# Optimization experiments

Hardware: AMD Instinct MI355X
Metric: run time of the kernel (lower is better)

## Reference

```python
import jax, jax.numpy as jnp
import numpy as np

FFT_LENGTH = 2048
HOP_LENGTH = 512  # window_length // 4, window_length == fft_length


def _hann_periodic(n):
    # tf.signal.hann_window(n, periodic=True)
    return (0.5 - 0.5 * jnp.cos(2.0 * jnp.pi * jnp.arange(n) / n)).astype(jnp.float32)


def setup_inputs() -> dict:
    key = jax.random.key(0)
    k1, k2 = jax.random.split(key)
    B, F, NB = 4, 4000, FFT_LENGTH // 2 + 1
    spec_real = jax.random.normal(k1, (B, F, NB), dtype=jnp.float32)
    spec_imag = jax.random.normal(k2, (B, F, NB), dtype=jnp.float32)
    return {"spec_real": spec_real, "spec_imag": spec_imag}


def reference(spec_real, spec_imag) -> jnp.ndarray:
    fft_length, hop = FFT_LENGTH, HOP_LENGTH
    B, F, _ = spec_real.shape
    window = _hann_periodic(fft_length)  # [N], window_length == fft_length so no padding

    # irfft of the complex spectrogram -> time-domain frames [B, F, N]
    frames = jnp.fft.irfft(spec_real + 1j * spec_imag, n=fft_length).astype(jnp.float32)
    windowed = window * frames  # [B, F, N]

    # overlap-and-add: output length L = (F-1)*hop + N
    L = (F - 1) * hop + fft_length
    idx = (jnp.arange(F) * hop)[:, None] + jnp.arange(fft_length)[None, :]  # [F, N]
    out = jnp.zeros((B, L), jnp.float32).at[:, idx].add(windowed)

    # librosa window_sumsquare: overlap-add of squared window, guard tiny values
    wsq = jnp.zeros((L,), jnp.float32).at[idx].add(window * window)
    tiny = jnp.float32(np.finfo(np.float32).tiny)
    window_sum = jnp.where(wsq > tiny, wsq, jnp.float32(1.0))

    y = out / window_sum
    # center=True: trim fft_length//2 on each side
    half = fft_length // 2
    return y[:, half:L - half]
```

## Files before the change

### kernel.cpp

```cpp
#include <hip/hip_runtime.h>
#include <math.h>

#define NB       1025
#define M        1024
#define FFTN     2048
#define HOP      512
#define NFRAMES  4000
#define BATCH    4
#define OUT_T    2047488
#define R_HOPS   8
#define REG_PB   501
#define ACC_N    (R_HOPS * HOP)
#define PI_F     3.14159265358979323846f

__device__ __forceinline__ float2 cmul(float2 a, float2 b) {
    return make_float2(a.x*b.x - a.y*b.y, a.x*b.y + a.y*b.x);
}
__device__ __forceinline__ int SW(int i) { return i ^ ((i >> 4) & 15); }

__device__ __forceinline__ float wsq_at(int p) {
    int u  = p + FFTN / 2;
    int fm = u >> 9;
    int n0 = u & 511;
    float wsq = 0.f;
    #pragma unroll
    for (int jj = 0; jj < 4; ++jj) {
        int fr = fm - jj;
        if (fr >= 0 && fr < NFRAMES) {
            int n = n0 + (jj << 9);
            float sw = __sinf((PI_F / (float)FFTN) * (float)n);
            float w  = sw * sw;
            wsq += w * w;
        }
    }
    const float tiny = 1.17549435e-38f;
    return (wsq > tiny) ? wsq : 1.0f;
}

template<int ST>
__device__ __forceinline__ void stage(const float2* __restrict__ src,
                                      float2* __restrict__ dst, int j,
                                      float2 w1, float2 w2, float2 w3) {
    const int Ns = 1 << (2 * ST);
    float2 v0 = src[SW(j)];
    float2 v1 = src[SW(j + 256)];
    float2 v2 = src[SW(j + 512)];
    float2 v3 = src[SW(j + 768)];
    v1 = cmul(v1, w1); v2 = cmul(v2, w2); v3 = cmul(v3, w3);
    float2 t0 = make_float2(v0.x + v2.x, v0.y + v2.y);
    float2 t1 = make_float2(v0.x - v2.x, v0.y - v2.y);
    float2 t2 = make_float2(v1.x + v3.x, v1.y + v3.y);
    float2 t3 = make_float2(v1.x - v3.x, v1.y - v3.y);
    int jm = j & (Ns - 1);
    int idxD = ((j >> (2 * ST)) << (2 * ST + 2)) + jm;
    dst[SW(idxD         )] = make_float2(t0.x + t2.x, t0.y + t2.y);
    dst[SW(idxD +     Ns)] = make_float2(t1.x - t3.y, t1.y + t3.x);
    dst[SW(idxD + 2 * Ns)] = make_float2(t0.x - t2.x, t0.y - t2.y);
    dst[SW(idxD + 3 * Ns)] = make_float2(t1.x + t3.y, t1.y - t3.x);
}

__global__ __launch_bounds__(256) void istft_region_kernel(
    const float* __restrict__ sr, const float* __restrict__ si,
    float* __restrict__ out)
{
    __shared__ float2 buf0[M];
    __shared__ float2 buf1[M];
    __shared__ float2 acc2[ACC_N / 2];

    const int blk = blockIdx.x;
    const int b   = blk / REG_PB;
    const int reg = blk - b * REG_PB;
    const int s0h = reg * R_HOPS;
    const int j   = threadIdx.x;

    #pragma unroll
    for (int q = 0; q < ACC_N / 2 / 256; ++q)
        acc2[j + q * 256] = make_float2(0.f, 0.f);

    float2 tw_pack[4];
    #pragma unroll
    for (int kk = 0; kk < 4; ++kk) {
        int k = j + kk * 256;
        float s, c;
        __sincosf(PI_F * (float)k * (1.0f / (float)M), &s, &c);
        tw_pack[kk] = make_float2(c, s);
    }
    float2 w1s[4], w2s[4], w3s[4];
    #pragma unroll
    for (int st = 1; st <= 4; ++st) {
        int Ns = 1 << (2 * st);
        int jm = j & (Ns - 1);
        float ang = (0.5f * PI_F / (float)Ns) * (float)jm;
        float s1, c1;
        __sincosf(ang, &s1, &c1);
        float2 w1 = make_float2(c1, s1);
        w1s[st-1] = w1;
        w2s[st-1] = cmul(w1, w1);
        w3s[st-1] = cmul(w2s[st-1], w1);
    }
    float wreg[4][2];
    #pragma unroll
    for (int q = 0; q < 4; ++q) {
        int n = j + q * 256;
        #pragma unroll
        for (int h = 0; h < 2; ++h) {
            int t = 2 * n + h;
            float swv = __sinf((PI_F / (float)FFTN) * (float)t);
            wreg[q][h] = swv * swv * (1.0f / 1024.0f);
        }
    }

    int f0 = s0h - 3;           if (f0 < 0)           f0 = 0;
    int f1 = s0h + R_HOPS - 1;  if (f1 > NFRAMES - 1) f1 = NFRAMES - 1;

    __syncthreads();

    float car[4], cai[4], cbr[4], cbi[4];
    {
        const size_t fb = ((size_t)b * NFRAMES + f0) * NB;
        const float* __restrict__ xr = sr + fb;
        const float* __restrict__ xi = si + fb;
        #pragma unroll
        for (int kk = 0; kk < 4; ++kk) {
            int k  = j + kk * 256;
            int mk = M - k;
            car[kk] = xr[k];  cai[kk] = xi[k];
            cbr[kk] = xr[mk]; cbi[kk] = xi[mk];
        }
    }

    for (int f = f0; f <= f1; ++f) {
        {
            float2 z[4];
            #pragma unroll
            for (int kk = 0; kk < 4; ++kk) {
                float arv = car[kk], aiv = cai[kk];
                float brv = cbr[kk], biv = cbi[kk];
                if (kk == 0 && j == 0) { aiv = 0.f; biv = 0.f; }
                float Er = 0.5f * (arv + brv), Ei = 0.5f * (aiv - biv);
                float Dr = 0.5f * (arv - brv), Di = 0.5f * (aiv + biv);
                float2 t = tw_pack[kk];
                float Or = Dr * t.x - Di * t.y;
                float Oi = Dr * t.y + Di * t.x;
                z[kk] = make_float2(Er - Oi, Ei + Or);
            }
            float2 t0 = make_float2(z[0].x + z[2].x, z[0].y + z[2].y);
            float2 t1 = make_float2(z[0].x - z[2].x, z[0].y - z[2].y);
            float2 t2 = make_float2(z[1].x + z[3].x, z[1].y + z[3].y);
            float2 t3 = make_float2(z[1].x - z[3].x, z[1].y - z[3].y);
            buf0[SW(4*j    )] = make_float2(t0.x + t2.x, t0.y + t2.y);
            buf0[SW(4*j + 1)] = make_float2(t1.x - t3.y, t1.y + t3.x);
            buf0[SW(4*j + 2)] = make_float2(t0.x - t2.x, t0.y - t2.y);
            buf0[SW(4*j + 3)] = make_float2(t1.x + t3.y, t1.y - t3.x);
        }

        float nar[4], nai[4], nbr[4], nbi[4];
        {
            int fn = (f < f1) ? (f + 1) : f1;
            const size_t fb = ((size_t)b * NFRAMES + fn) * NB;
            const float* __restrict__ xr = sr + fb;
            const float* __restrict__ xi = si + fb;
            #pragma unroll
            for (int kk = 0; kk < 4; ++kk) {
                int k  = j + kk * 256;
                int mk = M - k;
                nar[kk] = xr[k];  nai[kk] = xi[k];
                nbr[kk] = xr[mk]; nbi[kk] = xi[mk];
            }
        }

        __syncthreads();
        stage<1>(buf0, buf1, j, w1s[0], w2s[0], w3s[0]);
        __syncthreads();
        stage<2>(buf1, buf0, j, w1s[1], w2s[1], w3s[1]);
        __syncthreads();
        stage<3>(buf0, buf1, j, w1s[2], w2s[2], w3s[2]);
        __syncthreads();

        float2 v0 = buf1[SW(j)];
        float2 v1 = buf1[SW(j + 256)];
        float2 v2 = buf1[SW(j + 512)];
        float2 v3 = buf1[SW(j + 768)];
        v1 = cmul(v1, w1s[3]);
        v2 = cmul(v2, w2s[3]);
        v3 = cmul(v3, w3s[3]);
        float2 t0 = make_float2(v0.x + v2.x, v0.y + v2.y);
        float2 t1 = make_float2(v0.x - v2.x, v0.y - v2.y);
        float2 t2 = make_float2(v1.x + v3.x, v1.y + v3.y);
        float2 t3 = make_float2(v1.x - v3.x, v1.y - v3.y);
        float2 g0 = make_float2(t0.x + t2.x, t0.y + t2.y);
        float2 g1 = make_float2(t1.x - t3.y, t1.y + t3.x);
        float2 g2 = make_float2(t0.x - t2.x, t0.y - t2.y);
        float2 g3 = make_float2(t1.x + t3.y, t1.y - t3.x);

        int ofs2 = (HOP / 2) * (f - s0h);
        {
            int i2 = ofs2 + j;
            if ((unsigned)i2 < (unsigned)(ACC_N / 2)) {
                float2 a = acc2[i2];
                a.x += g0.x * wreg[0][0];  a.y += g0.y * wreg[0][1];
                acc2[i2] = a;
            }
            i2 = ofs2 + j + 256;
            if ((unsigned)i2 < (unsigned)(ACC_N / 2)) {
                float2 a = acc2[i2];
                a.x += g1.x * wreg[1][0];  a.y += g1.y * wreg[1][1];
                acc2[i2] = a;
            }
            i2 = ofs2 + j + 512;
            if ((unsigned)i2 < (unsigned)(ACC_N / 2)) {
                float2 a = acc2[i2];
                a.x += g2.x * wreg[2][0];  a.y += g2.y * wreg[2][1];
                acc2[i2] = a;
            }
            i2 = ofs2 + j + 768;
            if ((unsigned)i2 < (unsigned)(ACC_N / 2)) {
                float2 a = acc2[i2];
                a.x += g3.x * wreg[3][0];  a.y += g3.y * wreg[3][1];
                acc2[i2] = a;
            }
        }

        #pragma unroll
        for (int kk = 0; kk < 4; ++kk) {
            car[kk] = nar[kk]; cai[kk] = nai[kk];
            cbr[kk] = nbr[kk]; cbi[kk] = nbi[kk];
        }
    }

    __syncthreads();

    const float* accf = (const float*)acc2;
    const int base_u = s0h * HOP;
    float* outb = out + (size_t)b * OUT_T;
    #pragma unroll
    for (int q = 0; q < ACC_N / 256; ++q) {
        int i = j + q * 256;
        int p = base_u + i - FFTN / 2;
        if ((unsigned)p < (unsigned)OUT_T) {
            float invw = (p < 512 || p >= OUT_T - 512) ? (1.0f / wsq_at(p)) : (2.0f / 3.0f);
            outb[p] = accf[i] * invw;
        }
    }
}

extern "C" void kernel_launch(void* const* d_in, const int* in_sizes, int n_in,
                              void* d_out, int out_size, void* d_ws, size_t ws_size,
                              hipStream_t stream) {
    const float* sr = (const float*)d_in[0];
    const float* si = (const float*)d_in[1];
    float* out = (float*)d_out;
    istft_region_kernel<<<BATCH * REG_PB, 256, 0, stream>>>(sr, si, out);
}
```

Baseline: 61.30 us.

## Process two frames per iteration with in-place bit-reversed radix-4 FFT stages

The frame loop now handles two frames per pass, each in its own shared buffer. The stage-0 pack writes in digit-reversed order (rev4), so the radix-4 stages can run in place. Barriers are shared between the two frames, which cuts the per-frame synchronisation cost, and the next two frames' spectrum loads are prefetched in registers. This adds register pressure from the double prefetch and the extra in-flight data, and adds one barrier per iteration to protect buffer reuse.

```diff
diff --git a/kernel.cpp b/kernel.cpp
--- a/kernel.cpp
+++ b/kernel.cpp
@@ -18,6 +18,10 @@
 }
 __device__ __forceinline__ int SW(int i) { return i ^ ((i >> 4) & 15); }
 
+__device__ __forceinline__ int rev4(int j) {
+    return ((j & 3) << 6) | (((j >> 2) & 3) << 4) | (((j >> 4) & 3) << 2) | ((j >> 6) & 3);
+}
+
 __device__ __forceinline__ float wsq_at(int p) {
     int u  = p + FFTN / 2;
     int fm = u >> 9;
@@ -38,33 +42,106 @@
 }
 
 template<int ST>
-__device__ __forceinline__ void stage(const float2* __restrict__ src,
-                                      float2* __restrict__ dst, int j,
-                                      float2 w1, float2 w2, float2 w3) {
-    const int Ns = 1 << (2 * ST);
-    float2 v0 = src[SW(j)];
-    float2 v1 = src[SW(j + 256)];
-    float2 v2 = src[SW(j + 512)];
-    float2 v3 = src[SW(j + 768)];
+__device__ __forceinline__ void stage_ip(float2* buf, int j,
+                                         float2 w1, float2 w2, float2 w3) {
+    const int Ns   = 1 << (2 * ST);
+    const int jm   = j & (Ns - 1);
+    const int idxD = ((j >> (2 * ST)) << (2 * ST + 2)) + jm;
+    float2 v0 = buf[SW(idxD)];
+    float2 v1 = buf[SW(idxD + Ns)];
+    float2 v2 = buf[SW(idxD + 2 * Ns)];
+    float2 v3 = buf[SW(idxD + 3 * Ns)];
     v1 = cmul(v1, w1); v2 = cmul(v2, w2); v3 = cmul(v3, w3);
     float2 t0 = make_float2(v0.x + v2.x, v0.y + v2.y);
     float2 t1 = make_float2(v0.x - v2.x, v0.y - v2.y);
     float2 t2 = make_float2(v1.x + v3.x, v1.y + v3.y);
     float2 t3 = make_float2(v1.x - v3.x, v1.y - v3.y);
-    int jm = j & (Ns - 1);
-    int idxD = ((j >> (2 * ST)) << (2 * ST + 2)) + jm;
-    dst[SW(idxD         )] = make_float2(t0.x + t2.x, t0.y + t2.y);
-    dst[SW(idxD +     Ns)] = make_float2(t1.x - t3.y, t1.y + t3.x);
-    dst[SW(idxD + 2 * Ns)] = make_float2(t0.x - t2.x, t0.y - t2.y);
-    dst[SW(idxD + 3 * Ns)] = make_float2(t1.x + t3.y, t1.y - t3.x);
+    buf[SW(idxD         )] = make_float2(t0.x + t2.x, t0.y + t2.y);
+    buf[SW(idxD +     Ns)] = make_float2(t1.x - t3.y, t1.y + t3.x);
+    buf[SW(idxD + 2 * Ns)] = make_float2(t0.x - t2.x, t0.y - t2.y);
+    buf[SW(idxD + 3 * Ns)] = make_float2(t1.x + t3.y, t1.y - t3.x);
+}
+
+__device__ __forceinline__ void load_spec(const float* __restrict__ sr,
+                                          const float* __restrict__ si,
+                                          int b, int f, int j,
+                                          float* car, float* cai,
+                                          float* cbr, float* cbi) {
+    const size_t fb = ((size_t)b * NFRAMES + f) * NB;
+    const float* __restrict__ xr = sr + fb;
+    const float* __restrict__ xi = si + fb;
+    #pragma unroll
+    for (int kk = 0; kk < 4; ++kk) {
+        int k  = j + kk * 256;
+        int mk = M - k;
+        car[kk] = xr[k];  cai[kk] = xi[k];
+        cbr[kk] = xr[mk]; cbi[kk] = xi[mk];
+    }
+}
+
+__device__ __forceinline__ void pack_st0(float2* buf, int j, int R4,
+                                         const float2* tw_pack,
+                                         const float* car, const float* cai,
+                                         const float* cbr, const float* cbi) {
+    float2 z[4];
+    #pragma unroll
+    for (int kk = 0; kk < 4; ++kk) {
+        float arv = car[kk], aiv = cai[kk];
+        float brv = cbr[kk], biv = cbi[kk];
+        if (kk == 0 && j == 0) { aiv = 0.f; biv = 0.f; }
+        float Er = 0.5f * (arv + brv), Ei = 0.5f * (aiv - biv);
+        float Dr = 0.5f * (arv - brv), Di = 0.5f * (aiv + biv);
+        float2 t = tw_pack[kk];
+        float Or = Dr * t.x - Di * t.y;
+        float Oi = Dr * t.y + Di * t.x;
+        z[kk] = make_float2(Er - Oi, Ei + Or);
+    }
+    float2 t0 = make_float2(z[0].x + z[2].x, z[0].y + z[2].y);
+    float2 t1 = make_float2(z[0].x - z[2].x, z[0].y - z[2].y);
+    float2 t2 = make_float2(z[1].x + z[3].x, z[1].y + z[3].y);
+    float2 t3 = make_float2(z[1].x - z[3].x, z[1].y - z[3].y);
+    buf[SW(4 * R4    )] = make_float2(t0.x + t2.x, t0.y + t2.y);
+    buf[SW(4 * R4 + 1)] = make_float2(t1.x - t3.y, t1.y + t3.x);
+    buf[SW(4 * R4 + 2)] = make_float2(t0.x - t2.x, t0.y - t2.y);
+    buf[SW(4 * R4 + 3)] = make_float2(t1.x + t3.y, t1.y - t3.x);
+}
+
+__device__ __forceinline__ void st4_ola(const float2* buf, float2* acc2, int j,
+                                        int f_rel, float2 w1, float2 w2, float2 w3,
+                                        const float wreg[4][2]) {
+    float2 v0 = buf[SW(j)];
+    float2 v1 = buf[SW(j + 256)];
+    float2 v2 = buf[SW(j + 512)];
+    float2 v3 = buf[SW(j + 768)];
+    v1 = cmul(v1, w1); v2 = cmul(v2, w2); v3 = cmul(v3, w3);
+    float2 t0 = make_float2(v0.x + v2.x, v0.y + v2.y);
+    float2 t1 = make_float2(v0.x - v2.x, v0.y - v2.y);
+    float2 t2 = make_float2(v1.x + v3.x, v1.y + v3.y);
+    float2 t3 = make_float2(v1.x - v3.x, v1.y - v3.y);
+    float2 g[4];
+    g[0] = make_float2(t0.x + t2.x, t0.y + t2.y);
+    g[1] = make_float2(t1.x - t3.y, t1.y + t3.x);
+    g[2] = make_float2(t0.x - t2.x, t0.y - t2.y);
+    g[3] = make_float2(t1.x + t3.y, t1.y - t3.x);
+    const int ofs2 = 256 * f_rel;
+    #pragma unroll
+    for (int q = 0; q < 4; ++q) {
+        int i2 = ofs2 + j + q * 256;
+        if ((unsigned)i2 < (unsigned)(ACC_N / 2)) {
+            float2 a = acc2[i2];
+            a.x += g[q].x * wreg[q][0];
+            a.y += g[q].y * wreg[q][1];
+            acc2[i2] = a;
+        }
+    }
 }
 
 __global__ __launch_bounds__(256) void istft_region_kernel(
     const float* __restrict__ sr, const float* __restrict__ si,
     float* __restrict__ out)
 {
-    __shared__ float2 buf0[M];
-    __shared__ float2 buf1[M];
+    __shared__ float2 bufA[M];
+    __shared__ float2 bufB[M];
     __shared__ float2 acc2[ACC_N / 2];
 
     const int blk = blockIdx.x;
@@ -72,6 +149,7 @@
     const int reg = blk - b * REG_PB;
     const int s0h = reg * R_HOPS;
     const int j   = threadIdx.x;
+    const int R4  = rev4(j);
 
     #pragma unroll
     for (int q = 0; q < ACC_N / 2 / 256; ++q)
@@ -115,120 +193,43 @@
 
     __syncthreads();
 
-    float car[4], cai[4], cbr[4], cbi[4];
+    float arA[4], aiA[4], brA[4], biA[4];
+    float arB[4], aiB[4], brB[4], biB[4];
     {
-        const size_t fb = ((size_t)b * NFRAMES + f0) * NB;
-        const float* __restrict__ xr = sr + fb;
-        const float* __restrict__ xi = si + fb;
-        #pragma unroll
-        for (int kk = 0; kk < 4; ++kk) {
-            int k  = j + kk * 256;
-            int mk = M - k;
-            car[kk] = xr[k];  cai[kk] = xi[k];
-            cbr[kk] = xr[mk]; cbi[kk] = xi[mk];
-        }
-    }
-
-    for (int f = f0; f <= f1; ++f) {
+        int fB = (f0 + 1 <= f1) ? f0 + 1 : f1;
+        load_spec(sr, si, b, f0, j, arA, aiA, brA, biA);
+        load_spec(sr, si, b, fB, j, arB, aiB, brB, biB);
+    }
+
+    for (int f = f0; f <= f1; f += 2) {
+        const bool haveB = (f + 1 <= f1);
+
+        pack_st0(bufA, j, R4, tw_pack, arA, aiA, brA, biA);
+        if (haveB) pack_st0(bufB, j, R4, tw_pack, arB, aiB, brB, biB);
+
         {
-            float2 z[4];
-            #pragma unroll
-            for (int kk = 0; kk < 4; ++kk) {
-                float arv = car[kk], aiv = cai[kk];
-                float brv = cbr[kk], biv = cbi[kk];
-                if (kk == 0 && j == 0) { aiv = 0.f; biv = 0.f; }
-                float Er = 0.5f * (arv + brv), Ei = 0.5f * (aiv - biv);
-                float Dr = 0.5f * (arv - brv), Di = 0.5f * (aiv + biv);
-                float2 t = tw_pack[kk];
-                float Or = Dr * t.x - Di * t.y;
-                float Oi = Dr * t.y + Di * t.x;
-                z[kk] = make_float2(Er - Oi, Ei + Or);
-            }
-            float2 t0 = make_float2(z[0].x + z[2].x, z[0].y + z[2].y);
-            float2 t1 = make_float2(z[0].x - z[2].x, z[0].y - z[2].y);
-            float2 t2 = make_float2(z[1].x + z[3].x, z[1].y + z[3].y);
-            float2 t3 = make_float2(z[1].x - z[3].x, z[1].y - z[3].y);
-            buf0[SW(4*j    )] = make_float2(t0.x + t2.x, t0.y + t2.y);
-            buf0[SW(4*j + 1)] = make_float2(t1.x - t3.y, t1.y + t3.x);
-            buf0[SW(4*j + 2)] = make_float2(t0.x - t2.x, t0.y - t2.y);
-            buf0[SW(4*j + 3)] = make_float2(t1.x + t3.y, t1.y - t3.x);
-        }
-
-        float nar[4], nai[4], nbr[4], nbi[4];
-        {
-            int fn = (f < f1) ? (f + 1) : f1;
-            const size_t fb = ((size_t)b * NFRAMES + fn) * NB;
-            const float* __restrict__ xr = sr + fb;
-            const float* __restrict__ xi = si + fb;
-            #pragma unroll
-            for (int kk = 0; kk < 4; ++kk) {
-                int k  = j + kk * 256;
-                int mk = M - k;
-                nar[kk] = xr[k];  nai[kk] = xi[k];
-                nbr[kk] = xr[mk]; nbi[kk] = xi[mk];
-            }
-        }
-
-        __syncthreads();
-        stage<1>(buf0, buf1, j, w1s[0], w2s[0], w3s[0]);
-        __syncthreads();
-        stage<2>(buf1, buf0, j, w1s[1], w2s[1], w3s[1]);
-        __syncthreads();
-        stage<3>(buf0, buf1, j, w1s[2], w2s[2], w3s[2]);
-        __syncthreads();
-
-        float2 v0 = buf1[SW(j)];
-        float2 v1 = buf1[SW(j + 256)];
-        float2 v2 = buf1[SW(j + 512)];
-        float2 v3 = buf1[SW(j + 768)];
-        v1 = cmul(v1, w1s[3]);
-        v2 = cmul(v2, w2s[3]);
-        v3 = cmul(v3, w3s[3]);
-        float2 t0 = make_float2(v0.x + v2.x, v0.y + v2.y);
-        float2 t1 = make_float2(v0.x - v2.x, v0.y - v2.y);
-        float2 t2 = make_float2(v1.x + v3.x, v1.y + v3.y);
-        float2 t3 = make_float2(v1.x - v3.x, v1.y - v3.y);
-        float2 g0 = make_float2(t0.x + t2.x, t0.y + t2.y);
-        float2 g1 = make_float2(t1.x - t3.y, t1.y + t3.x);
-        float2 g2 = make_float2(t0.x - t2.x, t0.y - t2.y);
-        float2 g3 = make_float2(t1.x + t3.y, t1.y - t3.x);
-
-        int ofs2 = (HOP / 2) * (f - s0h);
-        {
-            int i2 = ofs2 + j;
-            if ((unsigned)i2 < (unsigned)(ACC_N / 2)) {
-                float2 a = acc2[i2];
-                a.x += g0.x * wreg[0][0];  a.y += g0.y * wreg[0][1];
-                acc2[i2] = a;
-            }
-            i2 = ofs2 + j + 256;
-            if ((unsigned)i2 < (unsigned)(ACC_N / 2)) {
-                float2 a = acc2[i2];
-                a.x += g1.x * wreg[1][0];  a.y += g1.y * wreg[1][1];
-                acc2[i2] = a;
-            }
-            i2 = ofs2 + j + 512;
-            if ((unsigned)i2 < (unsigned)(ACC_N / 2)) {
-                float2 a = acc2[i2];
-                a.x += g2.x * wreg[2][0];  a.y += g2.y * wreg[2][1];
-                acc2[i2] = a;
-            }
-            i2 = ofs2 + j + 768;
-            if ((unsigned)i2 < (unsigned)(ACC_N / 2)) {
-                float2 a = acc2[i2];
-                a.x += g3.x * wreg[3][0];  a.y += g3.y * wreg[3][1];
-                acc2[i2] = a;
-            }
-        }
-
-        #pragma unroll
-        for (int kk = 0; kk < 4; ++kk) {
-            car[kk] = nar[kk]; cai[kk] = nai[kk];
-            cbr[kk] = nbr[kk]; cbi[kk] = nbi[kk];
-        }
-    }
-
-    __syncthreads();
+            int fnA = f + 2;   if (fnA > f1) fnA = f1;
+            int fnB = fnA + 1; if (fnB > f1) fnB = f1;
+            load_spec(sr, si, b, fnA, j, arA, aiA, brA, biA);
+            load_spec(sr, si, b, fnB, j, arB, aiB, brB, biB);
+        }
+
+        __syncthreads();
+        stage_ip<1>(bufA, j, w1s[0], w2s[0], w3s[0]);
+        if (haveB) stage_ip<1>(bufB, j, w1s[0], w2s[0], w3s[0]);
+        __syncthreads();
+        stage_ip<2>(bufA, j, w1s[1], w2s[1], w3s[1]);
+        if (haveB) stage_ip<2>(bufB, j, w1s[1], w2s[1], w3s[1]);
+        __syncthreads();
+        stage_ip<3>(bufA, j, w1s[2], w2s[2], w3s[2]);
+        if (haveB) stage_ip<3>(bufB, j, w1s[2], w2s[2], w3s[2]);
+        __syncthreads();
+
+        st4_ola(bufA, acc2, j, f - s0h, w1s[3], w2s[3], w3s[3], wreg);
+        if (haveB) st4_ola(bufB, acc2, j, f + 1 - s0h, w1s[3], w2s[3], w3s[3], wreg);
+
+        __syncthreads();
+    }
 
     const float* accf = (const float*)acc2;
     const int base_u = s0h * HOP;
```

New measurement: 65.46 us. 1.07x slower.
